# Kernel optimization log

Measured on AMD Instinct MI355X. Metric: run time of the kernel, lower is better.

The kernel has to match this reference:

```python
import jax, jax.numpy as jnp
import numpy as np

D_MODEL = 256
SELF_NHEAD = 8
ATT_NHEAD = 8
DFF = 1024
H2D, W2D = 40, 40
MAX_DIS = 7
WS = 2 * MAX_DIS + 1  # 15x15 local window
LOCAL_DIL = 1
GN_GROUPS = 32
EPS = 1e-5


def _ln(x, g, b):
    m = jnp.mean(x, -1, keepdims=True)
    v = jnp.var(x, -1, keepdims=True)
    return (x - m) * jax.lax.rsqrt(v + EPS) * g + b


def _mha_core(q, k, v, nh):
    # q,k,v: (L, B, C); Q scaled by 1/sqrt(head_dim) as in AOT MultiheadAttention
    Lq, B, C = q.shape
    hd = C // nh
    qh = (q / jnp.asarray(hd ** 0.5, q.dtype)).reshape(Lq, B, nh, hd).transpose(1, 2, 0, 3)
    kh = k.reshape(-1, B, nh, hd).transpose(1, 2, 0, 3)
    vh = v.reshape(-1, B, nh, hd).transpose(1, 2, 0, 3)
    attn = jax.nn.softmax(jnp.einsum('bhqd,bhkd->bhqk', qh, kh), axis=-1)
    o = jnp.einsum('bhqk,bhkd->bhqd', attn, vh)
    return o.transpose(2, 0, 1, 3).reshape(Lq, B, C)


def _unfold(x, ws, dil):
    # x: (N, C, H, W) -> (N, C, ws*ws, H, W) local windows (zero-padded)
    n, c, h, w = x.shape
    p = (ws // 2) * dil
    pat = jax.lax.conv_general_dilated_patches(
        x, (ws, ws), (1, 1), [(p, p), (p, p)], rhs_dilation=(dil, dil))
    return pat.reshape(n, c, ws * ws, h, w)


def _local_attn(q2, k2, v2, nh, ws, dil):
    # q2,k2,v2: (B, C, H, W); windowed attention over (2*max_dis+1)^2 neighborhood
    b, c, h, w = q2.shape
    hd = c // nh
    qh = (q2 / jnp.asarray(hd ** 0.5, q2.dtype)).reshape(b, nh, hd, h * w)
    uk = _unfold(k2, ws, dil).reshape(b, nh, hd, ws * ws, h * w)
    uv = _unfold(v2, ws, dil).reshape(b, nh, hd, ws * ws, h * w)
    valid = _unfold(jnp.ones((1, 1, h, w), q2.dtype), ws, dil).reshape(1, 1, ws * ws, h * w) > 0.5
    logits = jnp.einsum('bhdn,bhdwn->bhwn', qh, uk)
    logits = jnp.where(valid, logits, jnp.asarray(-1e9, logits.dtype))
    attn = jax.nn.softmax(logits, axis=2)
    o = jnp.einsum('bhwn,bhdwn->bhdn', attn, uv)
    return o.reshape(b, c, h * w).transpose(2, 0, 1)  # (HW, B, C)


def _seq_to_2d(x, h, w):
    l, b, c = x.shape
    return x.reshape(h, w, b, c).transpose(2, 3, 0, 1)  # (B, C, h, w)


def _block(tgt, curr_id_emb, self_pos,
           ln1_g, ln1_b, sa_wq, sa_bq, sa_wk, sa_bk, sa_wv, sa_bv, sa_wo, sa_bo,
           ln2_g, ln2_b, w_qv, b_qv, w_id, b_id, lt_wo, lt_bo, st_wo, st_bo,
           ln3_g, ln3_b, w1, b1, gn_g, gn_b, dw_k, w2, b2):
    h, w = H2D, W2D
    # --- self attention (global_dilation == 1) ---
    _t = _ln(tgt, ln1_g, ln1_b)
    qk_in = _t + self_pos
    q_ = qk_in @ sa_wq.T + sa_bq
    k_ = qk_in @ sa_wk.T + sa_bk
    v_ = _t @ sa_wv.T + sa_bv
    tgt2 = _mha_core(q_, k_, v_, SELF_NHEAD) @ sa_wo.T + sa_bo
    tgt = tgt + tgt2
    # --- QV projection + ID-gated KV fusion ---
    _t = _ln(tgt, ln2_g, ln2_b)
    qv = _t @ w_qv.T + b_qv
    curr_Q = qv[..., :D_MODEL]  # curr_K == curr_Q
    curr_V = qv[..., D_MODEL:]
    id_kv = curr_id_emb @ w_id.T + b_id
    id_k = id_kv[..., :ATT_NHEAD]
    id_v = id_kv[..., ATT_NHEAD:]
    L, B, C = curr_Q.shape
    hd = C // ATT_NHEAD
    global_K = (curr_Q.reshape(L, B, ATT_NHEAD, hd) * (1.0 + jnp.tanh(id_k))[..., None]).reshape(L, B, C)
    global_V = curr_V + id_v
    # --- long-term (global) attention, no input linear ---
    tgt2 = _mha_core(curr_Q, global_K, global_V, ATT_NHEAD) @ lt_wo.T + lt_bo
    # --- short-term (local windowed) attention ---
    lq = _seq_to_2d(curr_Q, h, w)
    lk = _seq_to_2d(global_K, h, w)
    lv = _seq_to_2d(global_V, h, w)
    tgt3 = _local_attn(lq, lk, lv, ATT_NHEAD, WS, LOCAL_DIL) @ st_wo.T + st_bo
    tgt = tgt + tgt2 + tgt3
    # --- FFN with GN + GELU + depthwise 5x5 conv (GNActDWConv2d) ---
    _t = _ln(tgt, ln3_g, ln3_b)
    x = _t @ w1.T + b1  # (L, B, DFF)
    x2 = _seq_to_2d(x, h, w)  # (B, DFF, h, w)
    xr = x2.reshape(B, GN_GROUPS, DFF // GN_GROUPS, h, w)
    m = xr.mean((2, 3, 4), keepdims=True)
    va = xr.var((2, 3, 4), keepdims=True)
    x2 = ((xr - m) * jax.lax.rsqrt(va + EPS)).reshape(B, DFF, h, w)
    x2 = x2 * gn_g[None, :, None, None] + gn_b[None, :, None, None]
    x2 = jax.nn.gelu(x2, approximate=False)
    x2 = jax.lax.conv_general_dilated(
        x2, dw_k, (1, 1), [(2, 2), (2, 2)], feature_group_count=DFF,
        dimension_numbers=('NCHW', 'OIHW', 'NCHW'))
    x = x2.reshape(B, DFF, h * w).transpose(2, 0, 1)
    tgt2 = x @ w2.T + b2
    return tgt + tgt2


def setup_inputs() -> dict:
    key = jax.random.key(0)
    ks = jax.random.split(key, 40)
    L = H2D * W2D
    B = 1
    C = D_MODEL
    w = lambda k, s: jax.random.normal(k, s, jnp.float32) * 0.02
    inp = {
        'tgt': jax.random.normal(ks[0], (L, B, C), jnp.float32),
        'curr_id_emb': jax.random.normal(ks[1], (L, B, C), jnp.float32),
        'self_pos': jax.random.normal(ks[2], (L, B, C), jnp.float32),
        'ln1_g': jnp.ones((C,), jnp.float32), 'ln1_b': jnp.zeros((C,), jnp.float32),
        'sa_wq': w(ks[3], (C, C)), 'sa_bq': jnp.zeros((C,), jnp.float32),
        'sa_wk': w(ks[4], (C, C)), 'sa_bk': jnp.zeros((C,), jnp.float32),
        'sa_wv': w(ks[5], (C, C)), 'sa_bv': jnp.zeros((C,), jnp.float32),
        'sa_wo': w(ks[6], (C, C)), 'sa_bo': jnp.zeros((C,), jnp.float32),
        'ln2_g': jnp.ones((C,), jnp.float32), 'ln2_b': jnp.zeros((C,), jnp.float32),
        'w_qv': w(ks[7], (2 * C, C)), 'b_qv': jnp.zeros((2 * C,), jnp.float32),
        'w_id': w(ks[8], (C + ATT_NHEAD, C)), 'b_id': jnp.zeros((C + ATT_NHEAD,), jnp.float32),
        'lt_wo': w(ks[9], (C, C)), 'lt_bo': jnp.zeros((C,), jnp.float32),
        'st_wo': w(ks[10], (C, C)), 'st_bo': jnp.zeros((C,), jnp.float32),
        'ln3_g': jnp.ones((C,), jnp.float32), 'ln3_b': jnp.zeros((C,), jnp.float32),
        'w1': w(ks[11], (DFF, C)), 'b1': jnp.zeros((DFF,), jnp.float32),
        'gn_g': jnp.ones((DFF,), jnp.float32), 'gn_b': jnp.zeros((DFF,), jnp.float32),
        'dw_k': w(ks[12], (DFF, 1, 5, 5)),
        'w2': w(ks[13], (C, DFF)), 'b2': jnp.zeros((C,), jnp.float32),
    }
    return inp


def reference(tgt, curr_id_emb, self_pos,
              ln1_g, ln1_b, sa_wq, sa_bq, sa_wk, sa_bk, sa_wv, sa_bv, sa_wo, sa_bo,
              ln2_g, ln2_b, w_qv, b_qv, w_id, b_id, lt_wo, lt_bo, st_wo, st_bo,
              ln3_g, ln3_b, w1, b1, gn_g, gn_b, dw_k, w2, b2):
    return _block(tgt, curr_id_emb, self_pos,
                  ln1_g, ln1_b, sa_wq, sa_bq, sa_wk, sa_bk, sa_wv, sa_bv, sa_wo, sa_bo,
                  ln2_g, ln2_b, w_qv, b_qv, w_id, b_id, lt_wo, lt_bo, st_wo, st_bo,
                  ln3_g, ln3_b, w1, b1, gn_g, gn_b, dw_k, w2, b2)
```

## Files before the change

### kernel.cpp

```cpp
#include <hip/hip_runtime.h>
#include <math.h>

#define L_SEQ 1600
#define CDIM 256
#define NH 8
#define HD 32
#define GRID_H 40
#define GRID_W 40
#define DFF_ 1024
#define WS_ 15
#define WIN 225
#define MAXD 7
#define SCALE_QK 0.17677669529663687f

typedef __attribute__((ext_vector_type(8))) short short8;
typedef __attribute__((ext_vector_type(4))) float f32x4;

__device__ __forceinline__ float waveReduceSum(float v) {
#pragma unroll
    for (int off = 32; off > 0; off >>= 1) v += __shfl_down(v, off, 64);
    return v;
}
__device__ __forceinline__ float blockReduceSum(float v, float* sh4) {
    v = waveReduceSum(v);
    int lane = threadIdx.x & 63, wid = threadIdx.x >> 6;
    __syncthreads();
    if (lane == 0) sh4[wid] = v;
    __syncthreads();
    return sh4[0] + sh4[1] + sh4[2] + sh4[3];
}

__device__ __forceinline__ unsigned short f2bf(float x) {
    union { float f; unsigned u; } v; v.f = x;
    unsigned r = (v.u + 0x7FFFu + ((v.u >> 16) & 1u)) >> 16;
    return (unsigned short)r;
}
__device__ __forceinline__ unsigned pkbf(float lo, float hi) {
    return (unsigned)f2bf(lo) | ((unsigned)f2bf(hi) << 16);
}

__global__ __launch_bounds__(256) void ln_kernel(const float* __restrict__ x,
                                                 const float* __restrict__ g,
                                                 const float* __restrict__ b,
                                                 const float* __restrict__ addin,
                                                 float* __restrict__ out,
                                                 float* __restrict__ out2) {
    __shared__ float sh4[4];
    int row = blockIdx.x;
    int c = threadIdx.x;
    float v = x[row * CDIM + c];
    float mean = blockReduceSum(v, sh4) * (1.0f / CDIM);
    float d = v - mean;
    float var = blockReduceSum(d * d, sh4) * (1.0f / CDIM);
    float y = d * rsqrtf(var + 1e-5f) * g[c] + b[c];
    out[row * CDIM + c] = y;
    if (out2) out2[row * CDIM + c] = y + addin[row * CDIM + c];
}

__global__ __launch_bounds__(256) void gemm_mfma(const float* __restrict__ A,
                                                 const float* __restrict__ W,
                                                 const float* __restrict__ bias,
                                                 const float* __restrict__ res,
                                                 float* __restrict__ C,
                                                 int M, int N, int K) {
    __shared__ unsigned short Al[2][4][64][8];
    __shared__ unsigned short Bl[2][4][64][8];
    int tid = threadIdx.x;
    int bm = blockIdx.y * 64, bn = blockIdx.x * 64;
    int lane = tid & 63, wave = tid >> 6;
    int wr = wave >> 1, wc = wave & 1;

    int srow = tid >> 3;
    int q = tid & 7;
    int e0 = (q & 1) * 4;

    f32x4 acc[2][2] = {};
    int nsteps = K >> 5;

    float4 ra[2], rb[2];
    {
        int k0 = 0;
#pragma unroll
        for (int r = 0; r < 2; ++r) {
            int row = srow + 32 * r;
            ra[r] = *(const float4*)(A + (bm + row) * K + k0 + 4 * q);
            int n = bn + row;
            rb[r] = (n < N) ? *(const float4*)(W + n * K + k0 + 4 * q)
                            : make_float4(0.f, 0.f, 0.f, 0.f);
        }
#pragma unroll
        for (int r = 0; r < 2; ++r) {
            int row = srow + 32 * r;
            int frag = (row >> 4), l = (row & 15) + 16 * (q >> 1);
            unsigned pa0 = ((unsigned)f2bf(ra[r].x)) | (((unsigned)f2bf(ra[r].y)) << 16);
            unsigned pa1 = ((unsigned)f2bf(ra[r].z)) | (((unsigned)f2bf(ra[r].w)) << 16);
            unsigned pb0 = ((unsigned)f2bf(rb[r].x)) | (((unsigned)f2bf(rb[r].y)) << 16);
            unsigned pb1 = ((unsigned)f2bf(rb[r].z)) | (((unsigned)f2bf(rb[r].w)) << 16);
            *(uint2*)&Al[0][frag][l][e0] = make_uint2(pa0, pa1);
            *(uint2*)&Bl[0][frag][l][e0] = make_uint2(pb0, pb1);
        }
    }
    __syncthreads();

    for (int s = 0; s < nsteps; ++s) {
        bool more = (s + 1) < nsteps;
        if (more) {
            int k0 = (s + 1) << 5;
#pragma unroll
            for (int r = 0; r < 2; ++r) {
                int row = srow + 32 * r;
                ra[r] = *(const float4*)(A + (bm + row) * K + k0 + 4 * q);
                int n = bn + row;
                rb[r] = (n < N) ? *(const float4*)(W + n * K + k0 + 4 * q)
                                : make_float4(0.f, 0.f, 0.f, 0.f);
            }
        }
        {
            int buf = s & 1;
            short8 af[2], bfr[2];
#pragma unroll
            for (int i = 0; i < 2; ++i) {
                af[i] = *(const short8*)&Al[buf][2 * wr + i][lane][0];
                bfr[i] = *(const short8*)&Bl[buf][2 * wc + i][lane][0];
            }
#pragma unroll
            for (int i = 0; i < 2; ++i)
#pragma unroll
                for (int j = 0; j < 2; ++j)
                    acc[i][j] = __builtin_amdgcn_mfma_f32_16x16x32_bf16(af[i], bfr[j], acc[i][j], 0, 0, 0);
        }
        if (more) {
            int buf = (s + 1) & 1;
#pragma unroll
            for (int r = 0; r < 2; ++r) {
                int row = srow + 32 * r;
                int frag = (row >> 4), l = (row & 15) + 16 * (q >> 1);
                unsigned pa0 = ((unsigned)f2bf(ra[r].x)) | (((unsigned)f2bf(ra[r].y)) << 16);
                unsigned pa1 = ((unsigned)f2bf(ra[r].z)) | (((unsigned)f2bf(ra[r].w)) << 16);
                unsigned pb0 = ((unsigned)f2bf(rb[r].x)) | (((unsigned)f2bf(rb[r].y)) << 16);
                unsigned pb1 = ((unsigned)f2bf(rb[r].z)) | (((unsigned)f2bf(rb[r].w)) << 16);
                *(uint2*)&Al[buf][frag][l][e0] = make_uint2(pa0, pa1);
                *(uint2*)&Bl[buf][frag][l][e0] = make_uint2(pb0, pb1);
            }
        }
        __syncthreads();
    }

#pragma unroll
    for (int j = 0; j < 2; ++j) {
        int col = bn + wc * 32 + j * 16 + (lane & 15);
        if (col >= N) continue;
        float bv = bias ? bias[col] : 0.f;
#pragma unroll
        for (int i = 0; i < 2; ++i) {
            int rbase = bm + wr * 32 + i * 16 + ((lane >> 4) << 2);
#pragma unroll
            for (int r = 0; r < 4; ++r) {
                int row = rbase + r;
                float v = acc[i][j][r] + bv;
                if (res) v += res[row * N + col];
                C[row * N + col] = v;
            }
        }
    }
    (void)M;
}

#define QBLK 32
#define KTJ 128
__global__ __launch_bounds__(256) void mha_mfma(const float* __restrict__ Q,
                                                const float* __restrict__ K,
                                                const float* __restrict__ V,
                                                float* __restrict__ O) {
    __shared__ unsigned short Kl[8][64][8];
    __shared__ unsigned short Vl[4][2][64][12];
    __shared__ float mred[4][2][16];
    __shared__ float lred[4][2][16];
    __shared__ float Osh[3][2][2][64][4];
    int h = blockIdx.y;
    int qbase = blockIdx.x * QBLK;
    int tid = threadIdx.x;
    int w = tid >> 6, lane = tid & 63;
    int g = lane >> 4, c = lane & 15;

    short8 qfrag[2];
#pragma unroll
    for (int qt = 0; qt < 2; ++qt) {
        const float* qp = Q + (qbase + qt * 16 + c) * CDIM + h * HD + g * 8;
        float4 f0 = *(const float4*)qp;
        float4 f1 = *(const float4*)(qp + 4);
        short8 s;
        s[0] = (short)f2bf(f0.x * SCALE_QK); s[1] = (short)f2bf(f0.y * SCALE_QK);
        s[2] = (short)f2bf(f0.z * SCALE_QK); s[3] = (short)f2bf(f0.w * SCALE_QK);
        s[4] = (short)f2bf(f1.x * SCALE_QK); s[5] = (short)f2bf(f1.y * SCALE_QK);
        s[6] = (short)f2bf(f1.z * SCALE_QK); s[7] = (short)f2bf(f1.w * SCALE_QK);
        qfrag[qt] = s;
    }

    float m[2] = { -INFINITY, -INFINITY };
    float l[2] = { 0.f, 0.f };
    f32x4 acc_o[2][2] = {};

    int jrow = tid >> 1;
    int dhalf = (tid & 1) * 16;
    int vjq = tid >> 3;
    int vdq = tid & 7;
    int vjr = 4 * vjq;
    int vd0 = 4 * vdq;
    int vjc = vjr >> 5, vdt = vd0 >> 4, vjg = (vjr & 31) >> 3, ve0 = vjr & 7;

    int src_lo = 16 * ((2 * g) & 3) + c;
    int src_hi = 16 * ((2 * g + 1) & 3) + c;
    bool hisel = (g >= 2);

    for (int t = 0; t < L_SEQ; t += KTJ) {
        {
            int j = t + jrow;
            float4 f0, f1, f2, f3;
            if (j < L_SEQ) {
                const float4* kp = (const float4*)(K + j * CDIM + h * HD + dhalf);
                f0 = kp[0]; f1 = kp[1]; f2 = kp[2]; f3 = kp[3];
            } else {
                f0 = f1 = f2 = f3 = make_float4(0.f, 0.f, 0.f, 0.f);
            }
            int jt = jrow >> 4;
            int laneA = (jrow & 15) + dhalf * 2;
            short8 s0, s1;
            s0[0]=f2bf(f0.x); s0[1]=f2bf(f0.y); s0[2]=f2bf(f0.z); s0[3]=f2bf(f0.w);
            s0[4]=f2bf(f1.x); s0[5]=f2bf(f1.y); s0[6]=f2bf(f1.z); s0[7]=f2bf(f1.w);
            s1[0]=f2bf(f2.x); s1[1]=f2bf(f2.y); s1[2]=f2bf(f2.z); s1[3]=f2bf(f2.w);
            s1[4]=f2bf(f3.x); s1[5]=f2bf(f3.y); s1[6]=f2bf(f3.z); s1[7]=f2bf(f3.w);
            *(short8*)&Kl[jt][laneA][0] = s0;
            *(short8*)&Kl[jt][laneA + 16][0] = s1;
        }
        {
            float4 r0, r1, r2, r3;
            int j0 = t + vjr;
            const float* vb = V + h * HD + vd0;
            r0 = (j0 + 0 < L_SEQ) ? *(const float4*)(vb + (j0 + 0) * CDIM) : make_float4(0,0,0,0);
            r1 = (j0 + 1 < L_SEQ) ? *(const float4*)(vb + (j0 + 1) * CDIM) : make_float4(0,0,0,0);
            r2 = (j0 + 2 < L_SEQ) ? *(const float4*)(vb + (j0 + 2) * CDIM) : make_float4(0,0,0,0);
            r3 = (j0 + 3 < L_SEQ) ? *(const float4*)(vb + (j0 + 3) * CDIM) : make_float4(0,0,0,0);
            float col[4][4] = {
                { r0.x, r1.x, r2.x, r3.x },
                { r0.y, r1.y, r2.y, r3.y },
                { r0.z, r1.z, r2.z, r3.z },
                { r0.w, r1.w, r2.w, r3.w } };
#pragma unroll
            for (int dd = 0; dd < 4; ++dd) {
                int laneV = ((vd0 + dd) & 15) + 16 * vjg;
                uint2 pk;
                pk.x = pkbf(col[dd][0], col[dd][1]);
                pk.y = pkbf(col[dd][2], col[dd][3]);
                *(uint2*)&Vl[vjc][vdt][laneV][ve0] = pk;
            }
        }
        __syncthreads();

        bool alive = (t + 32 * w) < L_SEQ;
        if (alive) {
            short8 kf0 = *(const short8*)&Kl[2 * w][lane][0];
            short8 kf1 = *(const short8*)&Kl[2 * w + 1][lane][0];
            f32x4 zero = { 0.f, 0.f, 0.f, 0.f };
            f32x4 s[2][2];
            s[0][0] = __builtin_amdgcn_mfma_f32_16x16x32_bf16(kf0, qfrag[0], zero, 0, 0, 0);
            s[0][1] = __builtin_amdgcn_mfma_f32_16x16x32_bf16(kf0, qfrag[1], zero, 0, 0, 0);
            s[1][0] = __builtin_amdgcn_mfma_f32_16x16x32_bf16(kf1, qfrag[0], zero, 0, 0, 0);
            s[1][1] = __builtin_amdgcn_mfma_f32_16x16x32_bf16(kf1, qfrag[1], zero, 0, 0, 0);

            short8 pfrag[2];
#pragma unroll
            for (int qt = 0; qt < 2; ++qt) {
                float mx = s[0][qt][0];
                mx = fmaxf(mx, s[0][qt][1]); mx = fmaxf(mx, s[0][qt][2]); mx = fmaxf(mx, s[0][qt][3]);
                mx = fmaxf(mx, s[1][qt][0]); mx = fmaxf(mx, s[1][qt][1]);
                mx = fmaxf(mx, s[1][qt][2]); mx = fmaxf(mx, s[1][qt][3]);
                mx = fmaxf(mx, __shfl_xor(mx, 16, 64));
                mx = fmaxf(mx, __shfl_xor(mx, 32, 64));
                float nm = fmaxf(m[qt], mx);
                float alpha = __expf(m[qt] - nm);
                m[qt] = nm;
                float p00 = __expf(s[0][qt][0] - nm), p01 = __expf(s[0][qt][1] - nm);
                float p02 = __expf(s[0][qt][2] - nm), p03 = __expf(s[0][qt][3] - nm);
                float p10 = __expf(s[1][qt][0] - nm), p11 = __expf(s[1][qt][1] - nm);
                float p12 = __expf(s[1][qt][2] - nm), p13 = __expf(s[1][qt][3] - nm);
                float ts = ((p00 + p01) + (p02 + p03)) + ((p10 + p11) + (p12 + p13));
                ts += __shfl_xor(ts, 16, 64);
                ts += __shfl_xor(ts, 32, 64);
                l[qt] = l[qt] * alpha + ts;
#pragma unroll
                for (int dt = 0; dt < 2; ++dt) {
                    acc_o[dt][qt][0] *= alpha; acc_o[dt][qt][1] *= alpha;
                    acc_o[dt][qt][2] *= alpha; acc_o[dt][qt][3] *= alpha;
                }
                unsigned w00 = pkbf(p00, p01), w01 = pkbf(p02, p03);
                unsigned w10 = pkbf(p10, p11), w11 = pkbf(p12, p13);
                unsigned a0 = __shfl(w00, src_lo, 64);
                unsigned a1 = __shfl(w10, src_lo, 64);
                unsigned b0 = __shfl(w01, src_lo, 64);
                unsigned b1 = __shfl(w11, src_lo, 64);
                unsigned c0 = __shfl(w00, src_hi, 64);
                unsigned c1 = __shfl(w10, src_hi, 64);
                unsigned d0 = __shfl(w01, src_hi, 64);
                unsigned d1 = __shfl(w11, src_hi, 64);
                union { short8 s8; unsigned u[4]; } P;
                P.u[0] = hisel ? a1 : a0;
                P.u[1] = hisel ? b1 : b0;
                P.u[2] = hisel ? c1 : c0;
                P.u[3] = hisel ? d1 : d0;
                pfrag[qt] = P.s8;
            }

            union { short8 s8; uint2 v[2]; } vf0u, vf1u;
            vf0u.v[0] = *(const uint2*)&Vl[w][0][lane][0];
            vf0u.v[1] = *(const uint2*)&Vl[w][0][lane][4];
            vf1u.v[0] = *(const uint2*)&Vl[w][1][lane][0];
            vf1u.v[1] = *(const uint2*)&Vl[w][1][lane][4];
            acc_o[0][0] = __builtin_amdgcn_mfma_f32_16x16x32_bf16(vf0u.s8, pfrag[0], acc_o[0][0], 0, 0, 0);
            acc_o[0][1] = __builtin_amdgcn_mfma_f32_16x16x32_bf16(vf0u.s8, pfrag[1], acc_o[0][1], 0, 0, 0);
            acc_o[1][0] = __builtin_amdgcn_mfma_f32_16x16x32_bf16(vf1u.s8, pfrag[0], acc_o[1][0], 0, 0, 0);
            acc_o[1][1] = __builtin_amdgcn_mfma_f32_16x16x32_bf16(vf1u.s8, pfrag[1], acc_o[1][1], 0, 0, 0);
        }
        __syncthreads();
    }

    if (g == 0) {
#pragma unroll
        for (int qt = 0; qt < 2; ++qt) { mred[w][qt][c] = m[qt]; lred[w][qt][c] = l[qt]; }
    }
    if (w > 0) {
#pragma unroll
        for (int dt = 0; dt < 2; ++dt)
#pragma unroll
            for (int qt = 0; qt < 2; ++qt)
                *(f32x4*)&Osh[w - 1][dt][qt][lane][0] = acc_o[dt][qt];
    }
    __syncthreads();
    if (w == 0) {
#pragma unroll
        for (int qt = 0; qt < 2; ++qt) {
            float m0_ = mred[0][qt][c], m1_ = mred[1][qt][c];
            float m2_ = mred[2][qt][c], m3_ = mred[3][qt][c];
            float M = fmaxf(fmaxf(m0_, m1_), fmaxf(m2_, m3_));
            float a0 = __expf(m0_ - M), a1 = __expf(m1_ - M);
            float a2 = __expf(m2_ - M), a3 = __expf(m3_ - M);
            float L = a0 * lred[0][qt][c] + a1 * lred[1][qt][c]
                    + a2 * lred[2][qt][c] + a3 * lred[3][qt][c];
            float inv = 1.f / L;
#pragma unroll
            for (int dt = 0; dt < 2; ++dt) {
                f32x4 o1 = *(const f32x4*)&Osh[0][dt][qt][lane][0];
                f32x4 o2 = *(const f32x4*)&Osh[1][dt][qt][lane][0];
                f32x4 o3 = *(const f32x4*)&Osh[2][dt][qt][lane][0];
                float4 r;
                r.x = (acc_o[dt][qt][0] * a0 + o1[0] * a1 + o2[0] * a2 + o3[0] * a3) * inv;
                r.y = (acc_o[dt][qt][1] * a0 + o1[1] * a1 + o2[1] * a2 + o3[1] * a3) * inv;
                r.z = (acc_o[dt][qt][2] * a0 + o1[2] * a1 + o2[2] * a2 + o3[2] * a3) * inv;
                r.w = (acc_o[dt][qt][3] * a0 + o1[3] * a1 + o2[3] * a2 + o3[3] * a3) * inv;
                *(float4*)(O + (qbase + qt * 16 + c) * CDIM + h * HD + dt * 16 + 4 * g) = r;
            }
        }
    }
}

__global__ __launch_bounds__(256, 1) void local_mfma(const float* __restrict__ Q,
                                                     const float* __restrict__ K,
                                                     const float* __restrict__ V,
                                                     float* __restrict__ O) {
    __shared__ unsigned short Kp[768 * 40];
    __shared__ unsigned short Vt[32 * 776];
    __shared__ float mred[4][3][16];
    __shared__ float lred[4][3][16];
    __shared__ float Osh[3][2][3][64][4];
    int y = blockIdx.x, h = blockIdx.y;
    int tid = threadIdx.x;
    int w = tid >> 6, lane = tid & 63;
    int g = lane >> 4, c = lane & 15;

#pragma unroll 4
    for (int rep = 0; rep < 24; ++rep) {
        int idx = rep * 256 + tid;
        int key = idx >> 3, dq = idx & 7;
        int ky = key / 48;
        int xx = key - 48 * ky;
        int yy = y + ky - 7;
        bool ok = (xx < 40) && (yy >= 0) && (yy < 40);
        float4 fk = make_float4(0.f, 0.f, 0.f, 0.f);
        float4 fv = make_float4(0.f, 0.f, 0.f, 0.f);
        if (ok) {
            int pos = (yy * 40 + xx) * CDIM + h * HD + 4 * dq;
            fk = *(const float4*)(K + pos);
            fv = *(const float4*)(V + pos);
        }
        *(uint2*)&Kp[key * 40 + 4 * dq] = make_uint2(pkbf(fk.x, fk.y), pkbf(fk.z, fk.w));
        int vb = (4 * dq) * 776 + key;
        Vt[vb] = f2bf(fv.x);
        Vt[vb + 776] = f2bf(fv.y);
        Vt[vb + 1552] = f2bf(fv.z);
        Vt[vb + 2328] = f2bf(fv.w);
    }

    short8 qfrag[3];
#pragma unroll
    for (int qt = 0; qt < 3; ++qt) {
        short8 s = { 0, 0, 0, 0, 0, 0, 0, 0 };
        int qx = qt * 16 + c;
        if (qx < 40) {
            const float* qp = Q + (y * 40 + qx) * CDIM + h * HD + g * 8;
            float4 f0 = *(const float4*)qp;
            float4 f1 = *(const float4*)(qp + 4);
            s[0] = (short)f2bf(f0.x * SCALE_QK); s[1] = (short)f2bf(f0.y * SCALE_QK);
            s[2] = (short)f2bf(f0.z * SCALE_QK); s[3] = (short)f2bf(f0.w * SCALE_QK);
            s[4] = (short)f2bf(f1.x * SCALE_QK); s[5] = (short)f2bf(f1.y * SCALE_QK);
            s[6] = (short)f2bf(f1.z * SCALE_QK); s[7] = (short)f2bf(f1.w * SCALE_QK);
        }
        qfrag[qt] = s;
    }
    __syncthreads();

    f32x4 sfr[12][3];
    const f32x4 zf = { 0.f, 0.f, 0.f, 0.f };
#pragma unroll
    for (int i = 0; i < 12; ++i) {
        int ky = 4 * w + i / 3;
        int fx = i % 3;
        short8 kf = *(const short8*)&Kp[(ky * 48 + fx * 16 + c) * 40 + 8 * g];
#pragma unroll
        for (int qt = 0; qt < 3; ++qt)
            sfr[i][qt] = __builtin_amdgcn_mfma_f32_16x16x32_bf16(kf, qfrag[qt], zf, 0, 0, 0);
    }

    float mw[3] = { -1e30f, -1e30f, -1e30f };
#pragma unroll
    for (int i = 0; i < 12; ++i) {
        int ky = 4 * w + i / 3, fx = i % 3;
        int yy = y + ky - 7;
        bool rowok = (yy >= 0) && (yy < 40);
        int xxb = fx * 16 + 4 * g;
#pragma unroll
        for (int qt = 0; qt < 3; ++qt) {
            int qx = qt * 16 + c;
#pragma unroll
            for (int r = 0; r < 4; ++r) {
                int xx = xxb + r;
                int dd = xx - qx;
                bool ok = rowok && (xx < 40) && (dd <= 7) && (dd >= -7);
                float v = ok ? sfr[i][qt][r] : -1e9f;
                sfr[i][qt][r] = v;
                mw[qt] = fmaxf(mw[qt], v);
            }
        }
    }
#pragma unroll
    for (int qt = 0; qt < 3; ++qt) {
        mw[qt] = fmaxf(mw[qt], __shfl_xor(mw[qt], 16, 64));
        mw[qt] = fmaxf(mw[qt], __shfl_xor(mw[qt], 32, 64));
    }
    if (lane < 16) {
#pragma unroll
        for (int qt = 0; qt < 3; ++qt) mred[w][qt][lane] = mw[qt];
    }
    __syncthreads();
    float M[3];
#pragma unroll
    for (int qt = 0; qt < 3; ++qt)
        M[qt] = fmaxf(fmaxf(mred[0][qt][c], mred[1][qt][c]),
                      fmaxf(mred[2][qt][c], mred[3][qt][c]));

    float lsum[3] = { 0.f, 0.f, 0.f };
    f32x4 acc_o[2][3] = {};
    int src_lo = 16 * ((2 * g) & 3) + c;
    int src_hi = 16 * ((2 * g + 1) & 3) + c;
    bool hisel = (g >= 2);
#pragma unroll
    for (int chk = 0; chk < 6; ++chk) {
        short8 pfrag[3];
#pragma unroll
        for (int qt = 0; qt < 3; ++qt) {
            float p00 = __expf(sfr[2 * chk][qt][0] - M[qt]);
            float p01 = __expf(sfr[2 * chk][qt][1] - M[qt]);
            float p02 = __expf(sfr[2 * chk][qt][2] - M[qt]);
            float p03 = __expf(sfr[2 * chk][qt][3] - M[qt]);
            float p10 = __expf(sfr[2 * chk + 1][qt][0] - M[qt]);
            float p11 = __expf(sfr[2 * chk + 1][qt][1] - M[qt]);
            float p12 = __expf(sfr[2 * chk + 1][qt][2] - M[qt]);
            float p13 = __expf(sfr[2 * chk + 1][qt][3] - M[qt]);
            lsum[qt] += ((p00 + p01) + (p02 + p03)) + ((p10 + p11) + (p12 + p13));
            unsigned w00 = pkbf(p00, p01), w01 = pkbf(p02, p03);
            unsigned w10 = pkbf(p10, p11), w11 = pkbf(p12, p13);
            unsigned a0 = __shfl(w00, src_lo, 64);
            unsigned a1 = __shfl(w10, src_lo, 64);
            unsigned b0 = __shfl(w01, src_lo, 64);
            unsigned b1 = __shfl(w11, src_lo, 64);
            unsigned c0 = __shfl(w00, src_hi, 64);
            unsigned c1 = __shfl(w10, src_hi, 64);
            unsigned d0 = __shfl(w01, src_hi, 64);
            unsigned d1 = __shfl(w11, src_hi, 64);
            union { short8 s8; unsigned u[4]; } P;
            P.u[0] = hisel ? a1 : a0;
            P.u[1] = hisel ? b1 : b0;
            P.u[2] = hisel ? c1 : c0;
            P.u[3] = hisel ? d1 : d0;
            pfrag[qt] = P.s8;
        }
        int jb = 32 * (6 * w + chk);
        short8 vf0 = *(const short8*)&Vt[c * 776 + jb + 8 * g];
        short8 vf1 = *(const short8*)&Vt[(16 + c) * 776 + jb + 8 * g];
#pragma unroll
        for (int qt = 0; qt < 3; ++qt) {
            acc_o[0][qt] = __builtin_amdgcn_mfma_f32_16x16x32_bf16(vf0, pfrag[qt], acc_o[0][qt], 0, 0, 0);
            acc_o[1][qt] = __builtin_amdgcn_mfma_f32_16x16x32_bf16(vf1, pfrag[qt], acc_o[1][qt], 0, 0, 0);
        }
    }

#pragma unroll
    for (int qt = 0; qt < 3; ++qt) {
        lsum[qt] += __shfl_xor(lsum[qt], 16, 64);
        lsum[qt] += __shfl_xor(lsum[qt], 32, 64);
    }
    if (lane < 16) {
#pragma unroll
        for (int qt = 0; qt < 3; ++qt) lred[w][qt][lane] = lsum[qt];
    }
    if (w > 0) {
#pragma unroll
        for (int dt = 0; dt < 2; ++dt)
#pragma unroll
            for (int qt = 0; qt < 3; ++qt)
                *(f32x4*)&Osh[w - 1][dt][qt][lane][0] = acc_o[dt][qt];
    }
    __syncthreads();
    if (w == 0) {
#pragma unroll
        for (int qt = 0; qt < 3; ++qt) {
            int qx = qt * 16 + c;
            if (qx >= 40) continue;
            float L = (lred[0][qt][c] + lred[1][qt][c]) + (lred[2][qt][c] + lred[3][qt][c]);
            float inv = 1.f / L;
#pragma unroll
            for (int dt = 0; dt < 2; ++dt) {
                f32x4 o1 = *(const f32x4*)&Osh[0][dt][qt][lane][0];
                f32x4 o2 = *(const f32x4*)&Osh[1][dt][qt][lane][0];
                f32x4 o3 = *(const f32x4*)&Osh[2][dt][qt][lane][0];
                float4 r;
                r.x = (acc_o[dt][qt][0] + o1[0] + o2[0] + o3[0]) * inv;
                r.y = (acc_o[dt][qt][1] + o1[1] + o2[1] + o3[1]) * inv;
                r.z = (acc_o[dt][qt][2] + o1[2] + o2[2] + o3[2]) * inv;
                r.w = (acc_o[dt][qt][3] + o1[3] + o2[3] + o3[3]) * inv;
                *(float4*)(O + (y * 40 + qx) * CDIM + h * HD + dt * 16 + 4 * g) = r;
            }
        }
    }
}

__global__ __launch_bounds__(256) void make_qkv_kernel(const float* __restrict__ qv,
                                                       const float* __restrict__ idkv,
                                                       float* __restrict__ Qc,
                                                       float* __restrict__ gK,
                                                       float* __restrict__ gV) {
    int idx = blockIdx.x * 256 + threadIdx.x;
    if (idx >= L_SEQ * CDIM) return;
    int l = idx >> 8, c = idx & 255;
    int h = c >> 5;
    float q = qv[l * 512 + c];
    Qc[idx] = q;
    gK[idx] = q * (1.f + tanhf(idkv[l * 264 + h]));
    gV[idx] = qv[l * 512 + 256 + c] + idkv[l * 264 + 8 + c];
}

__global__ __launch_bounds__(256) void gn_partial(const float* __restrict__ X,
                                                  float* __restrict__ gstat) {
    __shared__ float sh4[4];
    int g = blockIdx.x, chunk = blockIdx.y;
    int base = g * 32;
    float s = 0.f, s2 = 0.f;
    for (int i = threadIdx.x; i < 200 * 32; i += 256) {
        int l = chunk * 200 + (i >> 5), c = i & 31;
        float v = X[l * DFF_ + base + c];
        s += v;
        s2 += v * v;
    }
    s = blockReduceSum(s, sh4);
    s2 = blockReduceSum(s2, sh4);
    if (threadIdx.x == 0) {
        gstat[g * 8 + chunk] = s;
        gstat[256 + g * 8 + chunk] = s2;
    }
}

__global__ __launch_bounds__(256) void gn_apply(const float* __restrict__ X,
                                                const float* __restrict__ gstat,
                                                const float* __restrict__ g,
                                                const float* __restrict__ b,
                                                float* __restrict__ Y) {
    int idx = blockIdx.x * 256 + threadIdx.x;
    int e4 = idx * 4;
    int c = e4 & 1023;
    int grp = c >> 5;
    float s = 0.f, s2 = 0.f;
#pragma unroll
    for (int i = 0; i < 8; ++i) {
        s += gstat[grp * 8 + i];
        s2 += gstat[256 + grp * 8 + i];
    }
    const float invn = 1.0f / 51200.f;
    float mean = s * invn;
    float rs = rsqrtf(s2 * invn - mean * mean + 1e-5f);
    float4 v = *(const float4*)(X + e4);
    float4 gg = *(const float4*)(g + c);
    float4 bb = *(const float4*)(b + c);
    float4 r;
    float y0 = (v.x - mean) * rs * gg.x + bb.x;
    float y1 = (v.y - mean) * rs * gg.y + bb.y;
    float y2 = (v.z - mean) * rs * gg.z + bb.z;
    float y3 = (v.w - mean) * rs * gg.w + bb.w;
    r.x = 0.5f * y0 * (1.0f + erff(y0 * 0.70710678118654752f));
    r.y = 0.5f * y1 * (1.0f + erff(y1 * 0.70710678118654752f));
    r.z = 0.5f * y2 * (1.0f + erff(y2 * 0.70710678118654752f));
    r.w = 0.5f * y3 * (1.0f + erff(y3 * 0.70710678118654752f));
    *(float4*)(Y + e4) = r;
}

__global__ __launch_bounds__(256) void dwk_transpose(const float* __restrict__ Kw,
                                                     float* __restrict__ Kt) {
    int idx = blockIdx.x * 256 + threadIdx.x;
    if (idx >= 25 * DFF_) return;
    int k = idx >> 10, c = idx & 1023;
    Kt[idx] = Kw[c * 25 + k];
}

__global__ __launch_bounds__(256) void dwconv_v2(const float* __restrict__ X,
                                                 const float* __restrict__ Kt,
                                                 float* __restrict__ Y) {
    int l = blockIdx.x;
    int c4 = threadIdx.x * 4;
    int y = l / GRID_W, x = l - y * GRID_W;
    float4 acc = make_float4(0.f, 0.f, 0.f, 0.f);
    if (y >= 2 && y < GRID_H - 2 && x >= 2 && x < GRID_W - 2) {
#pragma unroll
        for (int ky = 0; ky < 5; ++ky) {
#pragma unroll
            for (int kx = 0; kx < 5; ++kx) {
                float4 xv = *(const float4*)(X + ((y + ky - 2) * GRID_W + x + kx - 2) * DFF_ + c4);
                float4 wv = *(const float4*)(Kt + (ky * 5 + kx) * DFF_ + c4);
                acc.x += xv.x * wv.x; acc.y += xv.y * wv.y;
                acc.z += xv.z * wv.z; acc.w += xv.w * wv.w;
            }
        }
    } else {
#pragma unroll
        for (int ky = 0; ky < 5; ++ky) {
            int yy = y + ky - 2;
            if (yy < 0 || yy >= GRID_H) continue;
#pragma unroll
            for (int kx = 0; kx < 5; ++kx) {
                int xx = x + kx - 2;
                if (xx < 0 || xx >= GRID_W) continue;
                float4 xv = *(const float4*)(X + (yy * GRID_W + xx) * DFF_ + c4);
                float4 wv = *(const float4*)(Kt + (ky * 5 + kx) * DFF_ + c4);
                acc.x += xv.x * wv.x; acc.y += xv.y * wv.y;
                acc.z += xv.z * wv.z; acc.w += xv.w * wv.w;
            }
        }
    }
    *(float4*)(Y + l * DFF_ + c4) = acc;
}

extern "C" void kernel_launch(void* const* d_in, const int* in_sizes, int n_in,
                              void* d_out, int out_size, void* d_ws, size_t ws_size,
                              hipStream_t stream) {
    (void)in_sizes; (void)n_in; (void)out_size; (void)ws_size;
    const float* tgt = (const float*)d_in[0];
    const float* curr_id_emb = (const float*)d_in[1];
    const float* self_pos = (const float*)d_in[2];
    const float* ln1_g = (const float*)d_in[3];
    const float* ln1_b = (const float*)d_in[4];
    const float* sa_wq = (const float*)d_in[5];
    const float* sa_bq = (const float*)d_in[6];
    const float* sa_wk = (const float*)d_in[7];
    const float* sa_bk = (const float*)d_in[8];
    const float* sa_wv = (const float*)d_in[9];
    const float* sa_bv = (const float*)d_in[10];
    const float* sa_wo = (const float*)d_in[11];
    const float* sa_bo = (const float*)d_in[12];
    const float* ln2_g = (const float*)d_in[13];
    const float* ln2_b = (const float*)d_in[14];
    const float* w_qv = (const float*)d_in[15];
    const float* b_qv = (const float*)d_in[16];
    const float* w_id = (const float*)d_in[17];
    const float* b_id = (const float*)d_in[18];
    const float* lt_wo = (const float*)d_in[19];
    const float* lt_bo = (const float*)d_in[20];
    const float* st_wo = (const float*)d_in[21];
    const float* st_bo = (const float*)d_in[22];
    const float* ln3_g = (const float*)d_in[23];
    const float* ln3_b = (const float*)d_in[24];
    const float* w1 = (const float*)d_in[25];
    const float* b1 = (const float*)d_in[26];
    const float* gn_g = (const float*)d_in[27];
    const float* gn_b = (const float*)d_in[28];
    const float* dw_k = (const float*)d_in[29];
    const float* w2 = (const float*)d_in[30];
    const float* b2 = (const float*)d_in[31];
    float* out = (float*)d_out;

    float* ws = (float*)d_ws;
    const int LC = L_SEQ * CDIM;
    float* bufA = ws;
    float* bufB = bufA + LC;
    float* bufC = bufB + LC;
    float* bufD = bufC + LC;
    float* bufE = bufD + LC;
    float* bufF = bufE + LC;
    float* bufG = bufF + LC;
    float* bufH = bufG + LC;
    float* bufI = bufH + L_SEQ * 512;
    float* bufX = bufI + L_SEQ * 264;
    float* bufY = bufX + L_SEQ * DFF_;
    float* bufZ = bufY + L_SEQ * DFF_;
    float* bufW = bufZ + L_SEQ * DFF_;

    dim3 blk(256);
    dim3 g256(4, 25), g264(5, 25), g512(8, 25), g1024(16, 25);
    dim3 mhaGrid(L_SEQ / QBLK, NH);

    dwk_transpose<<<100, blk, 0, stream>>>(dw_k, bufW);
    ln_kernel<<<L_SEQ, blk, 0, stream>>>(tgt, ln1_g, ln1_b, self_pos, bufA, bufB);
    gemm_mfma<<<g256, blk, 0, stream>>>(bufB, sa_wq, sa_bq, nullptr, bufC, L_SEQ, CDIM, CDIM);
    gemm_mfma<<<g256, blk, 0, stream>>>(bufB, sa_wk, sa_bk, nullptr, bufD, L_SEQ, CDIM, CDIM);
    gemm_mfma<<<g256, blk, 0, stream>>>(bufA, sa_wv, sa_bv, nullptr, bufE, L_SEQ, CDIM, CDIM);
    mha_mfma<<<mhaGrid, blk, 0, stream>>>(bufC, bufD, bufE, bufF);
    gemm_mfma<<<g256, blk, 0, stream>>>(bufF, sa_wo, sa_bo, tgt, bufG, L_SEQ, CDIM, CDIM);
    ln_kernel<<<L_SEQ, blk, 0, stream>>>(bufG, ln2_g, ln2_b, nullptr, bufA, nullptr);
    gemm_mfma<<<g512, blk, 0, stream>>>(bufA, w_qv, b_qv, nullptr, bufH, L_SEQ, 512, CDIM);
    gemm_mfma<<<g264, blk, 0, stream>>>(curr_id_emb, w_id, b_id, nullptr, bufI, L_SEQ, 264, CDIM);
    make_qkv_kernel<<<L_SEQ, blk, 0, stream>>>(bufH, bufI, bufC, bufD, bufE);
    mha_mfma<<<mhaGrid, blk, 0, stream>>>(bufC, bufD, bufE, bufF);
    gemm_mfma<<<g256, blk, 0, stream>>>(bufF, lt_wo, lt_bo, bufG, bufB, L_SEQ, CDIM, CDIM);
    local_mfma<<<dim3(GRID_H, NH), blk, 0, stream>>>(bufC, bufD, bufE, bufF);
    gemm_mfma<<<g256, blk, 0, stream>>>(bufF, st_wo, st_bo, bufB, bufG, L_SEQ, CDIM, CDIM);
    ln_kernel<<<L_SEQ, blk, 0, stream>>>(bufG, ln3_g, ln3_b, nullptr, bufA, nullptr);
    gemm_mfma<<<g1024, blk, 0, stream>>>(bufA, w1, b1, nullptr, bufX, L_SEQ, DFF_, CDIM);
    gn_partial<<<dim3(32, 8), blk, 0, stream>>>(bufX, bufH);
    gn_apply<<<L_SEQ, blk, 0, stream>>>(bufX, bufH, gn_g, gn_b, bufY);
    dwconv_v2<<<L_SEQ, blk, 0, stream>>>(bufY, bufW, bufZ);
    gemm_mfma<<<g256, blk, 0, stream>>>(bufZ, w2, b2, bufG, out, L_SEQ, CDIM, DFF_);
}
```

Baseline: 383.5 us.

## Batch independent GEMMs via grid z and merge lt/st output projections

The GEMM kernel now takes up to three job descriptors selected by blockIdx.z, so the Q/K/V projections and the QV/ID projections each run as one launch instead of several. The long-term and short-term attention outputs are written side by side into a 512-wide buffer, and a prep kernel concatenates lt_wo/st_wo and sums their biases, so a single K=512 GEMM replaces two K=256 output projections. This cuts launch count and lets small GEMMs fill more of the GPU, at the cost of an extra weight-prep kernel and a longer K loop in the merged GEMM.

```diff
diff --git a/kernel.cpp b/kernel.cpp
--- a/kernel.cpp
+++ b/kernel.cpp
@@ -8,9 +8,6 @@
 #define GRID_H 40
 #define GRID_W 40
 #define DFF_ 1024
-#define WS_ 15
-#define WIN 225
-#define MAXD 7
 #define SCALE_QK 0.17677669529663687f
 
 typedef __attribute__((ext_vector_type(8))) short short8;
@@ -57,16 +54,27 @@
     if (out2) out2[row * CDIM + c] = y + addin[row * CDIM + c];
 }
 
-__global__ __launch_bounds__(256) void gemm_mfma(const float* __restrict__ A,
-                                                 const float* __restrict__ W,
-                                                 const float* __restrict__ bias,
-                                                 const float* __restrict__ res,
-                                                 float* __restrict__ C,
-                                                 int M, int N, int K) {
+struct GJob {
+    const float* A; const float* W; const float* bias; const float* res;
+    float* C; int N; int K;
+};
+
+__global__ __launch_bounds__(256) void gemm_mfma(GJob j0, GJob j1, GJob j2) {
+    GJob j = j0;
+    if (blockIdx.z == 1) j = j1;
+    else if (blockIdx.z == 2) j = j2;
+    const float* __restrict__ A = j.A;
+    const float* __restrict__ W = j.W;
+    const float* bias = j.bias;
+    const float* res = j.res;
+    float* __restrict__ C = j.C;
+    int N = j.N, K = j.K;
+
     __shared__ unsigned short Al[2][4][64][8];
     __shared__ unsigned short Bl[2][4][64][8];
     int tid = threadIdx.x;
     int bm = blockIdx.y * 64, bn = blockIdx.x * 64;
+    if (bn >= N) return;
     int lane = tid & 63, wave = tid >> 6;
     int wr = wave >> 1, wc = wave & 1;
 
@@ -79,25 +87,20 @@
 
     float4 ra[2], rb[2];
     {
-        int k0 = 0;
 #pragma unroll
         for (int r = 0; r < 2; ++r) {
             int row = srow + 32 * r;
-            ra[r] = *(const float4*)(A + (bm + row) * K + k0 + 4 * q);
+            ra[r] = *(const float4*)(A + (bm + row) * K + 4 * q);
             int n = bn + row;
-            rb[r] = (n < N) ? *(const float4*)(W + n * K + k0 + 4 * q)
+            rb[r] = (n < N) ? *(const float4*)(W + n * K + 4 * q)
                             : make_float4(0.f, 0.f, 0.f, 0.f);
         }
 #pragma unroll
         for (int r = 0; r < 2; ++r) {
             int row = srow + 32 * r;
             int frag = (row >> 4), l = (row & 15) + 16 * (q >> 1);
-            unsigned pa0 = ((unsigned)f2bf(ra[r].x)) | (((unsigned)f2bf(ra[r].y)) << 16);
-            unsigned pa1 = ((unsigned)f2bf(ra[r].z)) | (((unsigned)f2bf(ra[r].w)) << 16);
-            unsigned pb0 = ((unsigned)f2bf(rb[r].x)) | (((unsigned)f2bf(rb[r].y)) << 16);
-            unsigned pb1 = ((unsigned)f2bf(rb[r].z)) | (((unsigned)f2bf(rb[r].w)) << 16);
-            *(uint2*)&Al[0][frag][l][e0] = make_uint2(pa0, pa1);
-            *(uint2*)&Bl[0][frag][l][e0] = make_uint2(pb0, pb1);
+            *(uint2*)&Al[0][frag][l][e0] = make_uint2(pkbf(ra[r].x, ra[r].y), pkbf(ra[r].z, ra[r].w));
+            *(uint2*)&Bl[0][frag][l][e0] = make_uint2(pkbf(rb[r].x, rb[r].y), pkbf(rb[r].z, rb[r].w));
         }
     }
     __syncthreads();
@@ -126,8 +129,8 @@
 #pragma unroll
             for (int i = 0; i < 2; ++i)
 #pragma unroll
-                for (int j = 0; j < 2; ++j)
-                    acc[i][j] = __builtin_amdgcn_mfma_f32_16x16x32_bf16(af[i], bfr[j], acc[i][j], 0, 0, 0);
+                for (int jj = 0; jj < 2; ++jj)
+                    acc[i][jj] = __builtin_amdgcn_mfma_f32_16x16x32_bf16(af[i], bfr[jj], acc[i][jj], 0, 0, 0);
         }
         if (more) {
             int buf = (s + 1) & 1;
@@ -135,20 +138,16 @@
             for (int r = 0; r < 2; ++r) {
                 int row = srow + 32 * r;
                 int frag = (row >> 4), l = (row & 15) + 16 * (q >> 1);
-                unsigned pa0 = ((unsigned)f2bf(ra[r].x)) | (((unsigned)f2bf(ra[r].y)) << 16);
-                unsigned pa1 = ((unsigned)f2bf(ra[r].z)) | (((unsigned)f2bf(ra[r].w)) << 16);
-                unsigned pb0 = ((unsigned)f2bf(rb[r].x)) | (((unsigned)f2bf(rb[r].y)) << 16);
-                unsigned pb1 = ((unsigned)f2bf(rb[r].z)) | (((unsigned)f2bf(rb[r].w)) << 16);
-                *(uint2*)&Al[buf][frag][l][e0] = make_uint2(pa0, pa1);
-                *(uint2*)&Bl[buf][frag][l][e0] = make_uint2(pb0, pb1);
+                *(uint2*)&Al[buf][frag][l][e0] = make_uint2(pkbf(ra[r].x, ra[r].y), pkbf(ra[r].z, ra[r].w));
+                *(uint2*)&Bl[buf][frag][l][e0] = make_uint2(pkbf(rb[r].x, rb[r].y), pkbf(rb[r].z, rb[r].w));
             }
         }
         __syncthreads();
     }
 
 #pragma unroll
-    for (int j = 0; j < 2; ++j) {
-        int col = bn + wc * 32 + j * 16 + (lane & 15);
+    for (int jj = 0; jj < 2; ++jj) {
+        int col = bn + wc * 32 + jj * 16 + (lane & 15);
         if (col >= N) continue;
         float bv = bias ? bias[col] : 0.f;
 #pragma unroll
@@ -157,13 +156,12 @@
 #pragma unroll
             for (int r = 0; r < 4; ++r) {
                 int row = rbase + r;
-                float v = acc[i][j][r] + bv;
+                float v = acc[i][jj][r] + bv;
                 if (res) v += res[row * N + col];
                 C[row * N + col] = v;
             }
         }
     }
-    (void)M;
 }
 
 #define QBLK 32
@@ -171,7 +169,7 @@
 __global__ __launch_bounds__(256) void mha_mfma(const float* __restrict__ Q,
                                                 const float* __restrict__ K,
                                                 const float* __restrict__ V,
-                                                float* __restrict__ O) {
+                                                float* __restrict__ O, int ldo) {
     __shared__ unsigned short Kl[8][64][8];
     __shared__ unsigned short Vl[4][2][64][12];
     __shared__ float mred[4][2][16];
@@ -215,10 +213,10 @@
 
     for (int t = 0; t < L_SEQ; t += KTJ) {
         {
-            int j = t + jrow;
+            int jj = t + jrow;
             float4 f0, f1, f2, f3;
-            if (j < L_SEQ) {
-                const float4* kp = (const float4*)(K + j * CDIM + h * HD + dhalf);
+            if (jj < L_SEQ) {
+                const float4* kp = (const float4*)(K + jj * CDIM + h * HD + dhalf);
                 f0 = kp[0]; f1 = kp[1]; f2 = kp[2]; f3 = kp[3];
             } else {
                 f0 = f1 = f2 = f3 = make_float4(0.f, 0.f, 0.f, 0.f);
@@ -357,7 +355,7 @@
                 r.y = (acc_o[dt][qt][1] * a0 + o1[1] * a1 + o2[1] * a2 + o3[1] * a3) * inv;
                 r.z = (acc_o[dt][qt][2] * a0 + o1[2] * a1 + o2[2] * a2 + o3[2] * a3) * inv;
                 r.w = (acc_o[dt][qt][3] * a0 + o1[3] * a1 + o2[3] * a2 + o3[3] * a3) * inv;
-                *(float4*)(O + (qbase + qt * 16 + c) * CDIM + h * HD + dt * 16 + 4 * g) = r;
+                *(float4*)(O + (qbase + qt * 16 + c) * ldo + h * HD + dt * 16 + 4 * g) = r;
             }
         }
     }
@@ -366,7 +364,7 @@
 __global__ __launch_bounds__(256, 1) void local_mfma(const float* __restrict__ Q,
                                                      const float* __restrict__ K,
                                                      const float* __restrict__ V,
-                                                     float* __restrict__ O) {
+                                                     float* __restrict__ O, int ldo) {
     __shared__ unsigned short Kp[768 * 40];
     __shared__ unsigned short Vt[32 * 776];
     __shared__ float mred[4][3][16];
@@ -547,7 +545,7 @@
                 r.y = (acc_o[dt][qt][1] + o1[1] + o2[1] + o3[1]) * inv;
                 r.z = (acc_o[dt][qt][2] + o1[2] + o2[2] + o3[2]) * inv;
                 r.w = (acc_o[dt][qt][3] + o1[3] + o2[3] + o3[3]) * inv;
-                *(float4*)(O + (y * 40 + qx) * CDIM + h * HD + dt * 16 + 4 * g) = r;
+                *(float4*)(O + (y * 40 + qx) * ldo + h * HD + dt * 16 + 4 * g) = r;
             }
         }
     }
@@ -566,6 +564,19 @@
     Qc[idx] = q;
     gK[idx] = q * (1.f + tanhf(idkv[l * 264 + h]));
     gV[idx] = qv[l * 512 + 256 + c] + idkv[l * 264 + 8 + c];
+}
+
+__global__ __launch_bounds__(256) void prep_ltst(const float* __restrict__ lt_wo,
+                                                 const float* __restrict__ lt_bo,
+                                                 const float* __restrict__ st_wo,
+                                                 const float* __restrict__ st_bo,
+                                                 float* __restrict__ wcat,
+                                                 float* __restrict__ bsum) {
+    int idx = blockIdx.x * 256 + threadIdx.x;
+    int n = idx >> 8, k = idx & 255;
+    wcat[n * 512 + k] = lt_wo[idx];
+    wcat[n * 512 + 256 + k] = st_wo[idx];
+    if (idx < 256) bsum[idx] = lt_bo[idx] + st_bo[idx];
 }
 
 __global__ __launch_bounds__(256) void gn_partial(const float* __restrict__ X,
@@ -711,38 +722,62 @@
     float* bufC = bufB + LC;
     float* bufD = bufC + LC;
     float* bufE = bufD + LC;
-    float* bufF = bufE + LC;
-    float* bufG = bufF + LC;
-    float* bufH = bufG + LC;
+    float* bufG = bufE + LC;
+    float* bufFW = bufG + LC;
+    float* bufH = bufFW + L_SEQ * 512;
     float* bufI = bufH + L_SEQ * 512;
     float* bufX = bufI + L_SEQ * 264;
     float* bufY = bufX + L_SEQ * DFF_;
     float* bufZ = bufY + L_SEQ * DFF_;
     float* bufW = bufZ + L_SEQ * DFF_;
+    float* wcat = bufW + 25 * DFF_;
+    float* bsum = wcat + 256 * 512;
 
     dim3 blk(256);
-    dim3 g256(4, 25), g264(5, 25), g512(8, 25), g1024(16, 25);
     dim3 mhaGrid(L_SEQ / QBLK, NH);
+    auto J = [](const float* A, const float* W, const float* bias, const float* res,
+                float* C, int N, int K) {
+        GJob j; j.A = A; j.W = W; j.bias = bias; j.res = res; j.C = C; j.N = N; j.K = K;
+        return j;
+    };
 
     dwk_transpose<<<100, blk, 0, stream>>>(dw_k, bufW);
+    prep_ltst<<<256, blk, 0, stream>>>(lt_wo, lt_bo, st_wo, st_bo, wcat, bsum);
     ln_kernel<<<L_SEQ, blk, 0, stream>>>(tgt, ln1_g, ln1_b, self_pos, bufA, bufB);
-    gemm_mfma<<<g256, blk, 0, stream>>>(bufB, sa_wq, sa_bq, nullptr, bufC, L_SEQ, CDIM, CDIM);
-    gemm_mfma<<<g256, blk, 0, stream>>>(bufB, sa_wk, sa_bk, nullptr, bufD, L_SEQ, CDIM, CDIM);
-    gemm_mfma<<<g256, blk, 0, stream>>>(bufA, sa_wv, sa_bv, nullptr, bufE, L_SEQ, CDIM, CDIM);
-    mha_mfma<<<mhaGrid, blk, 0, stream>>>(bufC, bufD, bufE, bufF);
-    gemm_mfma<<<g256, blk, 0, stream>>>(bufF, sa_wo, sa_bo, tgt, bufG, L_SEQ, CDIM, CDIM);
+    {
+        GJob jq = J(bufB, sa_wq, sa_bq, nullptr, bufC, CDIM, CDIM);
+        GJob jk = J(bufB, sa_wk, sa_bk, nullptr, bufD, CDIM, CDIM);
+        GJob jv = J(bufA, sa_wv, sa_bv, nullptr, bufE, CDIM, CDIM);
+        gemm_mfma<<<dim3(4, 25, 3), blk, 0, stream>>>(jq, jk, jv);
+    }
+    mha_mfma<<<mhaGrid, blk, 0, stream>>>(bufC, bufD, bufE, bufFW, CDIM);
+    {
+        GJob jo = J(bufFW, sa_wo, sa_bo, tgt, bufG, CDIM, CDIM);
+        gemm_mfma<<<dim3(4, 25, 1), blk, 0, stream>>>(jo, jo, jo);
+    }
     ln_kernel<<<L_SEQ, blk, 0, stream>>>(bufG, ln2_g, ln2_b, nullptr, bufA, nullptr);
-    gemm_mfma<<<g512, blk, 0, stream>>>(bufA, w_qv, b_qv, nullptr, bufH, L_SEQ, 512, CDIM);
-    gemm_mfma<<<g264, blk, 0, stream>>>(curr_id_emb, w_id, b_id, nullptr, bufI, L_SEQ, 264, CDIM);
+    {
+        GJob jqv = J(bufA, w_qv, b_qv, nullptr, bufH, 512, CDIM);
+        GJob jid = J(curr_id_emb, w_id, b_id, nullptr, bufI, 264, CDIM);
+        gemm_mfma<<<dim3(8, 25, 2), blk, 0, stream>>>(jqv, jid, jid);
+    }
     make_qkv_kernel<<<L_SEQ, blk, 0, stream>>>(bufH, bufI, bufC, bufD, bufE);
-    mha_mfma<<<mhaGrid, blk, 0, stream>>>(bufC, bufD, bufE, bufF);
-    gemm_mfma<<<g256, blk, 0, stream>>>(bufF, lt_wo, lt_bo, bufG, bufB, L_SEQ, CDIM, CDIM);
-    local_mfma<<<dim3(GRID_H, NH), blk, 0, stream>>>(bufC, bufD, bufE, bufF);
-    gemm_mfma<<<g256, blk, 0, stream>>>(bufF, st_wo, st_bo, bufB, bufG, L_SEQ, CDIM, CDIM);
-    ln_kernel<<<L_SEQ, blk, 0, stream>>>(bufG, ln3_g, ln3_b, nullptr, bufA, nullptr);
-    gemm_mfma<<<g1024, blk, 0, stream>>>(bufA, w1, b1, nullptr, bufX, L_SEQ, DFF_, CDIM);
+    mha_mfma<<<mhaGrid, blk, 0, stream>>>(bufC, bufD, bufE, bufFW, 512);
+    local_mfma<<<dim3(GRID_H, NH), blk, 0, stream>>>(bufC, bufD, bufE, bufFW + 256, 512);
+    {
+        GJob jm = J(bufFW, wcat, bsum, bufG, bufB, CDIM, 512);
+        gemm_mfma<<<dim3(4, 25, 1), blk, 0, stream>>>(jm, jm, jm);
+    }
+    ln_kernel<<<L_SEQ, blk, 0, stream>>>(bufB, ln3_g, ln3_b, nullptr, bufA, nullptr);
+    {
+        GJob jw1 = J(bufA, w1, b1, nullptr, bufX, DFF_, CDIM);
+        gemm_mfma<<<dim3(16, 25, 1), blk, 0, stream>>>(jw1, jw1, jw1);
+    }
     gn_partial<<<dim3(32, 8), blk, 0, stream>>>(bufX, bufH);
     gn_apply<<<L_SEQ, blk, 0, stream>>>(bufX, bufH, gn_g, gn_b, bufY);
     dwconv_v2<<<L_SEQ, blk, 0, stream>>>(bufY, bufW, bufZ);
-    gemm_mfma<<<g256, blk, 0, stream>>>(bufZ, w2, b2, bufG, out, L_SEQ, CDIM, DFF_);
-}
+    {
+        GJob jw2 = J(bufZ, w2, b2, bufB, out, CDIM, DFF_);
+        gemm_mfma<<<dim3(4, 25, 1), blk, 0, stream>>>(jw2, jw2, jw2);
+    }
+}
```

Result: faster. 348.5 us (-9.1%).
